# Kernel tuning notes

Hardware: AMD Instinct MI355X
Metric: run time of the kernel (lower is better)

## Reference

```python
import jax, jax.numpy as jnp
import numpy as np
import math

STAGE_NUM = 5
EPS = 1e-6

def _l2norm(a, axis):
    return a / (EPS + jnp.linalg.norm(a, axis=axis, keepdims=True))

def setup_inputs() -> dict:
    key = jax.random.key(0)
    k1, k2, k3, k4 = jax.random.split(key, 4)
    b, n, c, h, w, k, out_c = 4, 4, 256, 64, 64, 128, 256
    x = jax.random.normal(k1, (b, c, h, w), dtype=jnp.float32)
    querys = jax.random.normal(k2, (b * n, c, h, w), dtype=jnp.float32)
    # mu init: normal(0, sqrt(2/k)) then l2norm over channel dim
    mu0 = jax.random.normal(k3, (1, c, k), dtype=jnp.float32) * math.sqrt(2.0 / k)
    mu0 = _l2norm(mu0, axis=1)
    # conv weight: normal(0, sqrt(2/(kh*kw*out_c)))
    fan = 3 * 3 * out_c
    conv_w = jax.random.normal(k4, (out_c, 2 * c, 3, 3), dtype=jnp.float32) * math.sqrt(2.0 / fan)
    conv_b = jnp.zeros((out_c,), dtype=jnp.float32)
    return {"x": x, "querys": querys, "mu0": mu0, "conv_w": conv_w, "conv_b": conv_b, "n": n}

def reference(x, querys, mu0, conv_w, conv_b, n):
    b, c, h, w = x.shape
    k = mu0.shape[2]
    xf = x.reshape(b, c, h * w)                       # [b, c, L]
    mu = jnp.broadcast_to(mu0, (b, c, k))

    # EM iterations (torch.no_grad -> stop_gradient)
    def em_step(mu, _):
        z = jnp.einsum('bcl,bck->blk', xf, mu)        # [b, L, k]
        z = jax.nn.softmax(z, axis=2)
        z_ = z / (EPS + jnp.sum(z, axis=1, keepdims=True))
        mu = jnp.einsum('bcl,blk->bck', xf, z_)       # [b, c, k]
        mu = _l2norm(mu, axis=1)
        return mu, None
    mu, _ = jax.lax.scan(em_step, mu, None, length=STAGE_NUM)
    mu = jax.lax.stop_gradient(mu)

    org_query = querys                                 # [b*n, c, h, w]
    q = querys.reshape(b, n, c, h, w).transpose(0, 2, 1, 3, 4).reshape(b, c, n * h * w)
    q_z = jax.nn.softmax(jnp.einsum('bcl,bck->blk', q, mu), axis=2)  # [b, nL, k]
    q_z = jax.lax.stop_gradient(q_z)

    rec = jnp.einsum('bck,blk->bcl', mu, q_z)          # [b, c, n*h*w]
    rec = rec.reshape(b, c, n, h, w).transpose(0, 2, 1, 3, 4).reshape(b * n, c, h, w)

    cat = jnp.concatenate((org_query, rec), axis=1)    # [b*n, 2c, h, w]
    out = jax.lax.conv_general_dilated(
        cat, conv_w, window_strides=(1, 1), padding='SAME',
        dimension_numbers=('NCHW', 'OIHW', 'NCHW'))
    out = out + conv_b[None, :, None, None]
    return (out, mu)
```

## Files before the change

### kernel.cpp

```cpp
#include <hip/hip_runtime.h>
#include <hip/hip_bf16.h>

#define B   4
#define NN  4
#define C   256
#define HH  64
#define WW  64
#define L   4096
#define NL  16384
#define K   128
#define OC  256
#define IC2 512
#define EPSV 1e-6f
#define PW  66
#define PA  4356

typedef __hip_bfloat16 bf16;
typedef __attribute__((ext_vector_type(8))) __bf16 bf16x8;
typedef __attribute__((ext_vector_type(4))) float f32x4;

#define AS1(p) ((const __attribute__((address_space(1))) void*)(p))
#define AS3(p) ((__attribute__((address_space(3))) void*)(p))

__global__ void k_init(const float* __restrict__ mu0, float* __restrict__ mu_f,
                       bf16* __restrict__ mub) {
    int i = blockIdx.x * 256 + threadIdx.x;
    int rem = i & 32767;
    int k = rem >> 8, c = rem & 255;
    float v = mu0[c * 128 + k];
    mu_f[i] = v;
    mub[i]  = __float2bfloat16(v);
}

__global__ void k_prepx(const float* __restrict__ x, bf16* __restrict__ xb,
                        bf16* __restrict__ xt) {
    __shared__ float ld[64][65];
    int lt = blockIdx.x, ct = blockIdx.y, b = blockIdx.z;
    int t = threadIdx.x;
    #pragma unroll
    for (int i = 0; i < 16; i++) {
        int idx = t + i * 256;
        int ch = idx >> 6, xl = idx & 63;
        size_t a = ((size_t)b * C + ct * 64 + ch) * L + lt * 64 + xl;
        float v = x[a];
        ld[ch][xl] = v;
        xb[a] = __float2bfloat16(v);
    }
    __syncthreads();
    #pragma unroll
    for (int i = 0; i < 16; i++) {
        int idx = t + i * 256;
        int xl = idx >> 6, ch = idx & 63;
        xt[((size_t)b * L + lt * 64 + xl) * 256 + ct * 64 + ch] = __float2bfloat16(ld[ch][xl]);
    }
}

__global__ void k_prepq(const float* __restrict__ qy, bf16* __restrict__ P2) {
    __shared__ float ld[64][65];
    int y = blockIdx.x, ct = blockIdx.y, img = blockIdx.z;
    int t = threadIdx.x;
    #pragma unroll
    for (int i = 0; i < 16; i++) {
        int idx = t + i * 256;
        int ch = idx >> 6, xl = idx & 63;
        ld[ch][xl] = qy[((size_t)img * C + ct * 64 + ch) * L + y * WW + xl];
    }
    __syncthreads();
    #pragma unroll
    for (int i = 0; i < 16; i++) {
        int idx = t + i * 256;
        int xl = idx >> 6, ch = idx & 63;
        P2[((size_t)img * PA + (size_t)(y + 1) * PW + xl + 1) * 512 + ct * 64 + ch] =
            __float2bfloat16(ld[ch][xl]);
    }
}

__global__ void k_zborder(uint4* __restrict__ P2) {
    int pi = blockIdx.x, img = blockIdx.y, t = threadIdx.x;
    int y, x;
    if      (pi < 66)  { y = 0;        x = pi; }
    else if (pi < 132) { y = 65;       x = pi - 66; }
    else if (pi < 196) { y = pi - 131; x = 0; }
    else               { y = pi - 195; x = 65; }
    P2[((size_t)img * PA + (size_t)y * PW + x) * 64 + t] = uint4{0, 0, 0, 0};
}

__global__ void k_wprep(const float* __restrict__ cw, bf16* __restrict__ wb) {
    int idx = blockIdx.x * 256 + threadIdx.x;
    if (idx >= 9 * OC * IC2) return;
    int r  = idx / (OC * IC2);
    int oc = (idx / IC2) & 255;
    int ic = idx & 511;
    wb[idx] = __float2bfloat16(cw[((size_t)oc * IC2 + ic) * 9 + r]);
}

__global__ void __launch_bounds__(256) k_z(const bf16* __restrict__ xt,
                                           const bf16* __restrict__ mub,
                                           bf16* __restrict__ zt) {
    __shared__ __align__(16) char smem[12288];
    char* tA = smem;
    char* tB = smem + 8192;
    int t = threadIdx.x, w = t >> 6, lane = t & 63;
    int b = blockIdx.y, l0 = blockIdx.x * 64;
    const bf16* Ab = mub + (size_t)b * K * C;
    const bf16* Bb = xt + ((size_t)b * L + l0) * C;
    int srow = t >> 2, sseg = t & 3, aseg = sseg ^ (srow & 3);
    char* dA0 = tA + w * 1024;
    char* dA1 = tA + 4096 + w * 1024;
    char* dB  = tB + w * 1024;
    int aoff[8], boff;
    #pragma unroll
    for (int i = 0; i < 8; i++) {
        int rowA = i * 16 + (lane & 15);
        aoff[i] = rowA * 64 + (((lane >> 4) ^ (rowA & 3)) << 4);
    }
    { int rowB = w * 16 + (lane & 15);
      boff = rowB * 64 + (((lane >> 4) ^ (rowB & 3)) << 4); }
    f32x4 acc[8];
    #pragma unroll
    for (int i = 0; i < 8; i++) acc[i] = f32x4{0.f, 0.f, 0.f, 0.f};
    for (int s = 0; s < 8; s++) {
        int cb0 = s * 32 + aseg * 8;
        __syncthreads();
        __builtin_amdgcn_global_load_lds(AS1(Ab + (size_t)srow * C + cb0),        AS3(dA0), 16, 0, 0);
        __builtin_amdgcn_global_load_lds(AS1(Ab + (size_t)(srow + 64) * C + cb0), AS3(dA1), 16, 0, 0);
        __builtin_amdgcn_global_load_lds(AS1(Bb + (size_t)srow * C + cb0),        AS3(dB),  16, 0, 0);
        __syncthreads();
        bf16x8 bfr = *(bf16x8*)(tB + boff);
        #pragma unroll
        for (int i = 0; i < 8; i++) {
            bf16x8 af = *(bf16x8*)(tA + aoff[i]);
            acc[i] = __builtin_amdgcn_mfma_f32_16x16x32_bf16(af, bfr, acc[i], 0, 0, 0);
        }
    }
    float m = -1e30f;
    #pragma unroll
    for (int i = 0; i < 8; i++)
        #pragma unroll
        for (int r = 0; r < 4; r++) m = fmaxf(m, acc[i][r]);
    m = fmaxf(m, __shfl_xor(m, 16, 64));
    m = fmaxf(m, __shfl_xor(m, 32, 64));
    float ssum = 0.f;
    #pragma unroll
    for (int i = 0; i < 8; i++)
        #pragma unroll
        for (int r = 0; r < 4; r++) { acc[i][r] = __expf(acc[i][r] - m); ssum += acc[i][r]; }
    ssum += __shfl_xor(ssum, 16, 64);
    ssum += __shfl_xor(ssum, 32, 64);
    float inv = 1.f / ssum;
    int quad = lane >> 4, col = lane & 15;
    bf16* zb = zt + (size_t)b * K * L + l0 + w * 16 + col;
    #pragma unroll
    for (int i = 0; i < 8; i++)
        #pragma unroll
        for (int r = 0; r < 4; r++) {
            int k = i * 16 + quad * 4 + r;
            zb[(size_t)k * L] = __float2bfloat16(acc[i][r] * inv);
        }
}

__global__ void __launch_bounds__(256) k_mu(const bf16* __restrict__ zt,
                                            const bf16* __restrict__ xb,
                                            float* __restrict__ part) {
    __shared__ __align__(16) char smem[16384];
    char* tA = smem; char* tB = smem + 8192;
    int t = threadIdx.x, w = t >> 6, lane = t & 63;
    int ct = blockIdx.x, chunk = blockIdx.y, b = blockIdx.z;
    const bf16* Ab = zt + (size_t)b * K * L + chunk * 256;
    const bf16* Bb = xb + ((size_t)b * C + ct * 128) * L + chunk * 256;
    int srow = t >> 2, sseg = t & 3, aseg = sseg ^ (srow & 3);
    char* dA0 = tA + w * 1024; char* dA1 = tA + 4096 + w * 1024;
    char* dB0 = tB + w * 1024; char* dB1 = tB + 4096 + w * 1024;
    int wm = w >> 1, wn = w & 1;
    int aoff[4], boff[4];
    #pragma unroll
    for (int i = 0; i < 4; i++) {
        int rowA = wm * 64 + i * 16 + (lane & 15);
        aoff[i] = rowA * 64 + (((lane >> 4) ^ (rowA & 3)) << 4);
        int rowB = wn * 64 + i * 16 + (lane & 15);
        boff[i] = rowB * 64 + (((lane >> 4) ^ (rowB & 3)) << 4);
    }
    f32x4 acc[4][4];
    #pragma unroll
    for (int i = 0; i < 4; i++)
        #pragma unroll
        for (int j = 0; j < 4; j++) acc[i][j] = f32x4{0.f, 0.f, 0.f, 0.f};
    for (int s = 0; s < 8; s++) {
        int lb = s * 32 + aseg * 8;
        __syncthreads();
        __builtin_amdgcn_global_load_lds(AS1(Ab + (size_t)srow * L + lb),        AS3(dA0), 16, 0, 0);
        __builtin_amdgcn_global_load_lds(AS1(Ab + (size_t)(srow + 64) * L + lb), AS3(dA1), 16, 0, 0);
        __builtin_amdgcn_global_load_lds(AS1(Bb + (size_t)srow * L + lb),        AS3(dB0), 16, 0, 0);
        __builtin_amdgcn_global_load_lds(AS1(Bb + (size_t)(srow + 64) * L + lb), AS3(dB1), 16, 0, 0);
        __syncthreads();
        bf16x8 af[4], bfr[4];
        #pragma unroll
        for (int i = 0; i < 4; i++) af[i]  = *(bf16x8*)(tA + aoff[i]);
        #pragma unroll
        for (int j = 0; j < 4; j++) bfr[j] = *(bf16x8*)(tB + boff[j]);
        #pragma unroll
        for (int i = 0; i < 4; i++)
            #pragma unroll
            for (int j = 0; j < 4; j++)
                acc[i][j] = __builtin_amdgcn_mfma_f32_16x16x32_bf16(af[i], bfr[j], acc[i][j], 0, 0, 0);
    }
    float* pb = part + ((size_t)(b * 16 + chunk) * K) * C + ct * 128;
    int quad = lane >> 4, col = lane & 15;
    #pragma unroll
    for (int i = 0; i < 4; i++) {
        int k = wm * 64 + i * 16 + quad * 4;
        #pragma unroll
        for (int j = 0; j < 4; j++) {
            int c = wn * 64 + j * 16 + col;
            #pragma unroll
            for (int r = 0; r < 4; r++)
                pb[(size_t)(k + r) * C + c] = acc[i][j][r];
        }
    }
}

__global__ void k_norm(const float* __restrict__ part, float* __restrict__ mu_f,
                       bf16* __restrict__ mub, bf16* __restrict__ muT) {
    int b = blockIdx.x >> 7, k = blockIdx.x & 127, lane = threadIdx.x;
    float v[4] = {0.f, 0.f, 0.f, 0.f};
    for (int ch = 0; ch < 16; ch++) {
        const float* p = part + ((size_t)(b * 16 + ch) * K + k) * C;
        #pragma unroll
        for (int j = 0; j < 4; j++) v[j] += p[lane + j * 64];
    }
    float s = v[0]*v[0] + v[1]*v[1] + v[2]*v[2] + v[3]*v[3];
    for (int o = 32; o > 0; o >>= 1) s += __shfl_xor(s, o, 64);
    float r = 1.f / (EPSV + sqrtf(s));
    float* mf = mu_f + ((size_t)b * K + k) * C;
    bf16*  mb = mub  + ((size_t)b * K + k) * C;
    bf16*  mt = muT  + (size_t)b * C * K + k;
    #pragma unroll
    for (int j = 0; j < 4; j++) {
        float val = v[j] * r;
        int c = lane + j * 64;
        mf[c] = val;
        mb[c] = __float2bfloat16(val);
        mt[(size_t)c * K] = __float2bfloat16(val);
    }
}

__global__ void __launch_bounds__(256) k_qz(const bf16* __restrict__ P2,
                                            const bf16* __restrict__ mub,
                                            bf16* __restrict__ qz) {
    __shared__ __align__(16) char smem[12288];
    char* tA = smem;
    char* tB = smem + 4096;
    int t = threadIdx.x, w = t >> 6, lane = t & 63;
    int b = blockIdx.y, tile = blockIdx.x;
    int n = tile >> 6, y = tile & 63;
    int img = b * NN + n;
    const bf16* Ab = P2 + ((size_t)img * PA + (size_t)(y + 1) * PW + 1) * 512;
    const bf16* Bb = mub + (size_t)b * K * C;
    int srow = t >> 2, sseg = t & 3, aseg = sseg ^ (srow & 3);
    char* dA  = tA + w * 1024;
    char* dB0 = tB + w * 1024;
    char* dB1 = tB + 4096 + w * 1024;
    int boff[8], aoff;
    #pragma unroll
    for (int j = 0; j < 8; j++) {
        int rowB = j * 16 + (lane & 15);
        boff[j] = rowB * 64 + (((lane >> 4) ^ (rowB & 3)) << 4);
    }
    { int rowA = w * 16 + (lane & 15);
      aoff = rowA * 64 + (((lane >> 4) ^ (rowA & 3)) << 4); }
    f32x4 acc[8];
    #pragma unroll
    for (int j = 0; j < 8; j++) acc[j] = f32x4{0.f, 0.f, 0.f, 0.f};
    for (int s = 0; s < 8; s++) {
        int cb0 = s * 32 + aseg * 8;
        __syncthreads();
        __builtin_amdgcn_global_load_lds(AS1(Ab + (size_t)srow * 512 + cb0),      AS3(dA),  16, 0, 0);
        __builtin_amdgcn_global_load_lds(AS1(Bb + (size_t)srow * C + cb0),        AS3(dB0), 16, 0, 0);
        __builtin_amdgcn_global_load_lds(AS1(Bb + (size_t)(srow + 64) * C + cb0), AS3(dB1), 16, 0, 0);
        __syncthreads();
        bf16x8 af = *(bf16x8*)(tA + aoff);
        #pragma unroll
        for (int j = 0; j < 8; j++) {
            bf16x8 bfr = *(bf16x8*)(tB + boff[j]);
            acc[j] = __builtin_amdgcn_mfma_f32_16x16x32_bf16(af, bfr, acc[j], 0, 0, 0);
        }
    }
    int quad = lane >> 4, col = lane & 15;
    bf16* qb = qz + ((size_t)b * NL + n * L + y * WW + w * 16 + quad * 4) * K;
    #pragma unroll
    for (int r = 0; r < 4; r++) {
        float mm = acc[0][r];
        #pragma unroll
        for (int j = 1; j < 8; j++) mm = fmaxf(mm, acc[j][r]);
        mm = fmaxf(mm, __shfl_xor(mm, 1, 64));
        mm = fmaxf(mm, __shfl_xor(mm, 2, 64));
        mm = fmaxf(mm, __shfl_xor(mm, 4, 64));
        mm = fmaxf(mm, __shfl_xor(mm, 8, 64));
        float ss = 0.f;
        float e[8];
        #pragma unroll
        for (int j = 0; j < 8; j++) { e[j] = __expf(acc[j][r] - mm); ss += e[j]; }
        ss += __shfl_xor(ss, 1, 64);
        ss += __shfl_xor(ss, 2, 64);
        ss += __shfl_xor(ss, 4, 64);
        ss += __shfl_xor(ss, 8, 64);
        float inv = 1.f / ss;
        #pragma unroll
        for (int j = 0; j < 8; j++)
            qb[(size_t)r * K + j * 16 + col] = __float2bfloat16(e[j] * inv);
    }
}

__global__ void __launch_bounds__(256) k_rec(const bf16* __restrict__ qz,
                                             const bf16* __restrict__ muT,
                                             bf16* __restrict__ P2) {
    __shared__ __align__(16) char smem[16384];
    char* tA = smem; char* tB = smem + 8192;
    int t = threadIdx.x, w = t >> 6, lane = t & 63;
    int ct = blockIdx.x, lt = blockIdx.y, b = blockIdx.z;
    const bf16* Ab = qz + ((size_t)b * NL + lt * 128) * K;
    const bf16* Bb = muT + ((size_t)b * C + ct * 128) * K;
    int srow = t >> 2, sseg = t & 3, aseg = sseg ^ (srow & 3);
    char* dA0 = tA + w * 1024; char* dA1 = tA + 4096 + w * 1024;
    char* dB0 = tB + w * 1024; char* dB1 = tB + 4096 + w * 1024;
    int wm = w >> 1, wn = w & 1;
    int aoff[4], boff[4];
    #pragma unroll
    for (int i = 0; i < 4; i++) {
        int rowA = wm * 64 + i * 16 + (lane & 15);
        aoff[i] = rowA * 64 + (((lane >> 4) ^ (rowA & 3)) << 4);
        int rowB = wn * 64 + i * 16 + (lane & 15);
        boff[i] = rowB * 64 + (((lane >> 4) ^ (rowB & 3)) << 4);
    }
    f32x4 acc[4][4];
    #pragma unroll
    for (int i = 0; i < 4; i++)
        #pragma unroll
        for (int j = 0; j < 4; j++) acc[i][j] = f32x4{0.f, 0.f, 0.f, 0.f};
    for (int s = 0; s < 4; s++) {
        int kb = s * 32 + aseg * 8;
        __syncthreads();
        __builtin_amdgcn_global_load_lds(AS1(Ab + (size_t)srow * K + kb),        AS3(dA0), 16, 0, 0);
        __builtin_amdgcn_global_load_lds(AS1(Ab + (size_t)(srow + 64) * K + kb), AS3(dA1), 16, 0, 0);
        __builtin_amdgcn_global_load_lds(AS1(Bb + (size_t)srow * K + kb),        AS3(dB0), 16, 0, 0);
        __builtin_amdgcn_global_load_lds(AS1(Bb + (size_t)(srow + 64) * K + kb), AS3(dB1), 16, 0, 0);
        __syncthreads();
        bf16x8 af[4], bfr[4];
        #pragma unroll
        for (int i = 0; i < 4; i++) af[i]  = *(bf16x8*)(tA + aoff[i]);
        #pragma unroll
        for (int j = 0; j < 4; j++) bfr[j] = *(bf16x8*)(tB + boff[j]);
        #pragma unroll
        for (int i = 0; i < 4; i++)
            #pragma unroll
            for (int j = 0; j < 4; j++)
                acc[i][j] = __builtin_amdgcn_mfma_f32_16x16x32_bf16(af[i], bfr[j], acc[i][j], 0, 0, 0);
    }
    int quad = lane >> 4, col = lane & 15;
    #pragma unroll
    for (int i = 0; i < 4; i++) {
        int lbase = lt * 128 + wm * 64 + i * 16 + quad * 4;
        #pragma unroll
        for (int r = 0; r < 4; r++) {
            int l = lbase + r;
            int n = l >> 12, p = l & 4095;
            int y = p >> 6, xp = p & 63;
            bf16* dst = P2 + ((size_t)(b * NN + n) * PA + (size_t)(y + 1) * PW + xp + 1) * 512 + 256;
            #pragma unroll
            for (int j = 0; j < 4; j++)
                dst[ct * 128 + wn * 64 + j * 16 + col] = __float2bfloat16(acc[i][j][r]);
        }
    }
}

__global__ void __launch_bounds__(256) k_conv(const bf16* __restrict__ P2,
                                              const bf16* __restrict__ Wb,
                                              const float* __restrict__ cb,
                                              float* __restrict__ out) {
    __shared__ __align__(16) char smem[41472];
    char* inl = smem;
    char* wld = smem + 16896;
    int t = threadIdx.x, w = t >> 6, lane = t & 63;
    int m0  = blockIdx.x * 128;
    int y0  = blockIdx.y * 2;
    int img = blockIdx.z;
    int srow = t >> 2;
    int aseg = (t & 3) ^ ((srow ^ (srow >> 2)) & 3);
    int wm = w >> 1, wn = w & 1;
    int q = lane >> 4, lane15 = lane & 15;

    int aoff[4];
    #pragma unroll
    for (int i = 0; i < 4; i++) {
        int rowA = wm * 64 + i * 16 + lane15;
        aoff[i] = rowA * 64 + (((q ^ (rowA ^ (rowA >> 2))) & 3) << 4);
    }
    int pj0[4];
    #pragma unroll
    for (int j = 0; j < 4; j++) pj0[j] = j * 16 + lane15;

    auto stageIN = [&](int cc) {
        size_t rowb = ((size_t)img * PA + (size_t)(y0 + w) * PW) * 512 + cc * 32;
        #pragma unroll
        for (int it = 0; it < 4; it++) {
            int px = it * 16 + (lane >> 2);
            int sg = (lane & 3) ^ ((px ^ (px >> 1)) & 3);
            __builtin_amdgcn_global_load_lds(AS1(P2 + rowb + (size_t)px * 512 + sg * 8),
                AS3(inl + w * 4224 + it * 1024), 16, 0, 0);
        }
        if (lane < 8) {
            int px = 64 + (lane >> 2);
            int sg = (lane & 3) ^ ((px ^ (px >> 1)) & 3);
            __builtin_amdgcn_global_load_lds(AS1(P2 + rowb + (size_t)px * 512 + sg * 8),
                AS3(inl + w * 4224 + 4096), 16, 0, 0);
        }
    };

    f32x4 acc[4][4];
    #pragma unroll
    for (int i = 0; i < 4; i++) {
        int oc = m0 + wm * 64 + i * 16 + q * 4;
        #pragma unroll
        for (int r = 0; r < 4; r++) {
            float bv = cb[oc + r];
            #pragma unroll
            for (int j = 0; j < 4; j++) acc[i][j][r] = bv;
        }
    }

    stageIN(0);
    {
        const bf16* w0 = Wb + (size_t)(m0 + srow) * IC2 + aseg * 8;
        __builtin_amdgcn_global_load_lds(AS1(w0),                         AS3(wld + w * 1024), 16, 0, 0);
        __builtin_amdgcn_global_load_lds(AS1(w0 + (size_t)64 * IC2),      AS3(wld + 4096 + w * 1024), 16, 0, 0);
        const bf16* w1 = w0 + (size_t)(OC * IC2);
        __builtin_amdgcn_global_load_lds(AS1(w1),                         AS3(wld + 8192 + w * 1024), 16, 0, 0);
        __builtin_amdgcn_global_load_lds(AS1(w1 + (size_t)64 * IC2),      AS3(wld + 8192 + 4096 + w * 1024), 16, 0, 0);
    }
    asm volatile("s_waitcnt vmcnt(0)" ::: "memory");
    __builtin_amdgcn_s_barrier();
    asm volatile("" ::: "memory");

    for (int cc = 0; cc < 16; cc++) {
        #pragma unroll
        for (int rt = 0; rt < 9; rt++) {
            const int dy = rt / 3, dx = rt % 3;
            char* wbuf = wld + (rt % 3) * 8192;
            bf16x8 af[4], bfr[4];
            #pragma unroll
            for (int i = 0; i < 4; i++) af[i] = *(bf16x8*)(wbuf + aoff[i]);
            #pragma unroll
            for (int j = 0; j < 4; j++) {
                int p = pj0[j] + dx;
                bfr[j] = *(bf16x8*)(inl + (wn + dy) * 4224 + p * 64 +
                                    (((q ^ (p ^ (p >> 1))) & 3) << 4));
            }
            const bool doPf = (cc * 9 + rt + 2) < 144;
            if (doPf) {
                const int g2 = rt + 2;
                const int rt2 = (g2 >= 9) ? g2 - 9 : g2;
                const int cc2 = cc + (g2 >= 9 ? 1 : 0);
                char* wdst = wld + ((rt + 2) % 3) * 8192;
                const bf16* wsrc = Wb + (size_t)rt2 * (OC * IC2) + (size_t)(m0 + srow) * IC2
                                 + cc2 * 32 + aseg * 8;
                __builtin_amdgcn_global_load_lds(AS1(wsrc),                    AS3(wdst + w * 1024), 16, 0, 0);
                __builtin_amdgcn_global_load_lds(AS1(wsrc + (size_t)64 * IC2), AS3(wdst + 4096 + w * 1024), 16, 0, 0);
            }
            __builtin_amdgcn_s_setprio(1);
            #pragma unroll
            for (int i = 0; i < 4; i++)
                #pragma unroll
                for (int j = 0; j < 4; j++)
                    acc[i][j] = __builtin_amdgcn_mfma_f32_16x16x32_bf16(af[i], bfr[j], acc[i][j], 0, 0, 0);
            __builtin_amdgcn_s_setprio(0);
            if (rt == 8) {
                if (cc < 15) {
                    asm volatile("" ::: "memory");
                    __builtin_amdgcn_s_barrier();
                    asm volatile("" ::: "memory");
                    stageIN(cc + 1);
                    asm volatile("s_waitcnt vmcnt(0)" ::: "memory");
                    __builtin_amdgcn_s_barrier();
                    asm volatile("" ::: "memory");
                }
            } else {
                if (doPf) asm volatile("s_waitcnt vmcnt(2)" ::: "memory");
                else      asm volatile("s_waitcnt vmcnt(0)" ::: "memory");
                __builtin_amdgcn_s_barrier();
                asm volatile("" ::: "memory");
            }
        }
    }

    int pxbase = blockIdx.y * 128 + wn * 64 + lane15;
    #pragma unroll
    for (int i = 0; i < 4; i++) {
        int oc = m0 + wm * 64 + i * 16 + q * 4;
        #pragma unroll
        for (int j = 0; j < 4; j++) {
            int px = pxbase + j * 16;
            #pragma unroll
            for (int r = 0; r < 4; r++)
                out[((size_t)img * OC + oc + r) * L + px] = acc[i][j][r];
        }
    }
}

__global__ void k_muout(const float* __restrict__ mu_f, float* __restrict__ out) {
    int i = blockIdx.x * 256 + threadIdx.x;
    int b = i >> 15, rem = i & 32767;
    int c = rem >> 7, k = rem & 127;
    out[(size_t)16777216 + i] = mu_f[((size_t)b * K + k) * C + c];
}

extern "C" void kernel_launch(void* const* d_in, const int* in_sizes, int n_in,
                              void* d_out, int out_size, void* d_ws, size_t ws_size,
                              hipStream_t stream) {
    const float* x   = (const float*)d_in[0];
    const float* qy  = (const float*)d_in[1];
    const float* mu0 = (const float*)d_in[2];
    const float* cw  = (const float*)d_in[3];
    const float* cb  = (const float*)d_in[4];
    float* out = (float*)d_out;

    char* ws = (char*)d_ws;
    float* mu_f = (float*)(ws);
    bf16*  mu_b = (bf16*) (ws + 524288);
    bf16*  muT  = (bf16*) (ws + 786432);
    bf16*  Wb   = (bf16*) (ws + 1048576);
    bf16*  zt   = (bf16*) (ws + 3407872);
    bf16*  qz   = (bf16*) (ws + 3407872);
    bf16*  P2   = (bf16*) (ws + 20185088);
    bf16*  x_bf = (bf16*) (ws + 20185088);
    float* part = (float*)(ws + 20185088 + 8388608);
    bf16*  xt   = (bf16*) (ws + 20185088 + 16777216);

    k_init<<<512, 256, 0, stream>>>(mu0, mu_f, mu_b);
    k_prepx<<<dim3(64, 4, 4), 256, 0, stream>>>(x, x_bf, xt);

    for (int it = 0; it < 5; it++) {
        k_z<<<dim3(64, 4), 256, 0, stream>>>(xt, mu_b, zt);
        k_mu<<<dim3(2, 16, 4), 256, 0, stream>>>(zt, x_bf, part);
        k_norm<<<512, 64, 0, stream>>>(part, mu_f, mu_b, muT);
    }

    k_prepq<<<dim3(64, 4, 16), 256, 0, stream>>>(qy, P2);
    k_zborder<<<dim3(260, 16), 64, 0, stream>>>((uint4*)P2);
    k_wprep<<<4608, 256, 0, stream>>>(cw, Wb);

    k_qz<<<dim3(256, 4), 256, 0, stream>>>(P2, mu_b, qz);
    k_rec<<<dim3(2, 128, 4), 256, 0, stream>>>(qz, muT, P2);
    k_conv<<<dim3(2, 32, 16), 256, 0, stream>>>(P2, Wb, cb, out);
    k_muout<<<512, 256, 0, stream>>>(mu_f, out);
}
```

Measured before the change: 425.7 us.

## Double conv output tile to four rows per block to reuse weights

The implicit-GEMM conv block now covers four output rows (256 pixels) instead of two. Each wave holds a 4x8 accumulator grid, and B fragments are loaded inside the MFMA loop, so every weight fragment staged in LDS feeds twice as many MFMAs. This halves the grid and the weight traffic per output and amortises the per-tap barriers. The cost is more accumulator registers, a larger LDS input halo, and fewer blocks in flight.

```diff
diff --git a/kernel.cpp b/kernel.cpp
--- a/kernel.cpp
+++ b/kernel.cpp
@@ -373,16 +373,16 @@
     }
 }
 
-__global__ void __launch_bounds__(256) k_conv(const bf16* __restrict__ P2,
-                                              const bf16* __restrict__ Wb,
-                                              const float* __restrict__ cb,
-                                              float* __restrict__ out) {
-    __shared__ __align__(16) char smem[41472];
+__global__ void __launch_bounds__(256, 2) k_conv(const bf16* __restrict__ P2,
+                                                 const bf16* __restrict__ Wb,
+                                                 const float* __restrict__ cb,
+                                                 float* __restrict__ out) {
+    __shared__ __align__(16) char smem[49920];
     char* inl = smem;
-    char* wld = smem + 16896;
+    char* wld = smem + 25344;
     int t = threadIdx.x, w = t >> 6, lane = t & 63;
     int m0  = blockIdx.x * 128;
-    int y0  = blockIdx.y * 2;
+    int y0  = blockIdx.y * 4;
     int img = blockIdx.z;
     int srow = t >> 2;
     int aseg = (t & 3) ^ ((srow ^ (srow >> 2)) & 3);
@@ -395,28 +395,31 @@
         int rowA = wm * 64 + i * 16 + lane15;
         aoff[i] = rowA * 64 + (((q ^ (rowA ^ (rowA >> 2))) & 3) << 4);
     }
-    int pj0[4];
-    #pragma unroll
-    for (int j = 0; j < 4; j++) pj0[j] = j * 16 + lane15;
 
     auto stageIN = [&](int cc) {
-        size_t rowb = ((size_t)img * PA + (size_t)(y0 + w) * PW) * 512 + cc * 32;
-        #pragma unroll
-        for (int it = 0; it < 4; it++) {
-            int px = it * 16 + (lane >> 2);
-            int sg = (lane & 3) ^ ((px ^ (px >> 1)) & 3);
-            __builtin_amdgcn_global_load_lds(AS1(P2 + rowb + (size_t)px * 512 + sg * 8),
-                AS3(inl + w * 4224 + it * 1024), 16, 0, 0);
-        }
-        if (lane < 8) {
-            int px = 64 + (lane >> 2);
-            int sg = (lane & 3) ^ ((px ^ (px >> 1)) & 3);
-            __builtin_amdgcn_global_load_lds(AS1(P2 + rowb + (size_t)px * 512 + sg * 8),
-                AS3(inl + w * 4224 + 4096), 16, 0, 0);
+        size_t ibase = (size_t)img * PA * 512 + cc * 32;
+        #pragma unroll
+        for (int it = 0; it < 6; it++) {
+            unsigned g = it * 256 + t;
+            unsigned row = g / 264u, ps = g - row * 264u;
+            unsigned px = ps >> 2, s0 = ps & 3;
+            unsigned sg = s0 ^ ((px ^ (px >> 1)) & 3);
+            __builtin_amdgcn_global_load_lds(
+                AS1(P2 + ibase + ((size_t)(y0 + row) * PW + px) * 512 + sg * 8),
+                AS3(inl + it * 4096 + w * 1024), 16, 0, 0);
+        }
+        if (t < 48) {
+            unsigned g = 1536 + t;
+            unsigned row = g / 264u, ps = g - row * 264u;
+            unsigned px = ps >> 2, s0 = ps & 3;
+            unsigned sg = s0 ^ ((px ^ (px >> 1)) & 3);
+            __builtin_amdgcn_global_load_lds(
+                AS1(P2 + ibase + ((size_t)(y0 + row) * PW + px) * 512 + sg * 8),
+                AS3(inl + 24576), 16, 0, 0);
         }
     };
 
-    f32x4 acc[4][4];
+    f32x4 acc[4][8];
     #pragma unroll
     for (int i = 0; i < 4; i++) {
         int oc = m0 + wm * 64 + i * 16 + q * 4;
@@ -424,7 +427,7 @@
         for (int r = 0; r < 4; r++) {
             float bv = cb[oc + r];
             #pragma unroll
-            for (int j = 0; j < 4; j++) acc[i][j][r] = bv;
+            for (int j = 0; j < 8; j++) acc[i][j][r] = bv;
         }
     }
 
@@ -446,15 +449,9 @@
         for (int rt = 0; rt < 9; rt++) {
             const int dy = rt / 3, dx = rt % 3;
             char* wbuf = wld + (rt % 3) * 8192;
-            bf16x8 af[4], bfr[4];
+            bf16x8 af[4];
             #pragma unroll
             for (int i = 0; i < 4; i++) af[i] = *(bf16x8*)(wbuf + aoff[i]);
-            #pragma unroll
-            for (int j = 0; j < 4; j++) {
-                int p = pj0[j] + dx;
-                bfr[j] = *(bf16x8*)(inl + (wn + dy) * 4224 + p * 64 +
-                                    (((q ^ (p ^ (p >> 1))) & 3) << 4));
-            }
             const bool doPf = (cc * 9 + rt + 2) < 144;
             if (doPf) {
                 const int g2 = rt + 2;
@@ -468,10 +465,15 @@
             }
             __builtin_amdgcn_s_setprio(1);
             #pragma unroll
-            for (int i = 0; i < 4; i++)
+            for (int j = 0; j < 8; j++) {
+                int p = (j & 3) * 16 + lane15 + dx;
+                int rowsel = 2 * wn + (j >> 2) + dy;
+                bf16x8 bfr = *(bf16x8*)(inl + rowsel * 4224 + p * 64 +
+                                        (((q ^ (p ^ (p >> 1))) & 3) << 4));
                 #pragma unroll
-                for (int j = 0; j < 4; j++)
-                    acc[i][j] = __builtin_amdgcn_mfma_f32_16x16x32_bf16(af[i], bfr[j], acc[i][j], 0, 0, 0);
+                for (int i = 0; i < 4; i++)
+                    acc[i][j] = __builtin_amdgcn_mfma_f32_16x16x32_bf16(af[i], bfr, acc[i][j], 0, 0, 0);
+            }
             __builtin_amdgcn_s_setprio(0);
             if (rt == 8) {
                 if (cc < 15) {
@@ -492,13 +494,12 @@
         }
     }
 
-    int pxbase = blockIdx.y * 128 + wn * 64 + lane15;
     #pragma unroll
     for (int i = 0; i < 4; i++) {
         int oc = m0 + wm * 64 + i * 16 + q * 4;
         #pragma unroll
-        for (int j = 0; j < 4; j++) {
-            int px = pxbase + j * 16;
+        for (int j = 0; j < 8; j++) {
+            int px = blockIdx.y * 256 + wn * 128 + (j >> 2) * 64 + (j & 3) * 16 + lane15;
             #pragma unroll
             for (int r = 0; r < 4; r++)
                 out[((size_t)img * OC + oc + r) * L + px] = acc[i][j][r];
@@ -550,6 +551,6 @@
 
     k_qz<<<dim3(256, 4), 256, 0, stream>>>(P2, mu_b, qz);
     k_rec<<<dim3(2, 128, 4), 256, 0, stream>>>(qz, muT, P2);
-    k_conv<<<dim3(2, 32, 16), 256, 0, stream>>>(P2, Wb, cb, out);
+    k_conv<<<dim3(2, 16, 16), 256, 0, stream>>>(P2, Wb, cb, out);
     k_muout<<<512, 256, 0, stream>>>(mu_f, out);
 }
```

Measured after the change: 410.9 us. 1.04x faster.
